# Optimization experiments

Hardware: AMD Instinct MI355X
Metric: run time of the kernel (lower is better)

The kernel has to match this reference:

```python
import jax, jax.numpy as jnp
import numpy as np
from jax.scipy.linalg import cho_solve

N, D, T, K, P = 4000, 256, 52, 20, 100
EPS = 1e-8


def _make_kernel(length_scale):
    # RBF kernel over time grid with the same jitter-doubling rule as the torch code.
    t = np.arange(T, dtype=np.float32)
    sq = (t[None, :] - t[:, None]) ** 2
    Kmat = np.exp(-0.5 * sq / np.float32(length_scale) ** 2).astype(np.float32)
    jitter = 1e-4
    eye = np.eye(T, dtype=np.float32)
    while True:
        if np.linalg.cond(Kmat + jitter * eye) < 1e4:
            break
        jitter *= 2
        if jitter > 0.1:
            break
    return jnp.asarray(Kmat + jitter * eye)

K_LAMBDA = _make_kernel(T / 4)  # lambda GP kernel, shared across all k
K_PHI = _make_kernel(T / 3)     # phi GP kernel, shared across all k


def setup_inputs() -> dict:
    key = jax.random.key(0)
    ks = jax.random.split(key, 7)
    lambda_ = jax.random.normal(ks[0], (N, K, T), dtype=jnp.float32)
    phi = jax.random.normal(ks[1], (K, D, T), dtype=jnp.float32)
    gamma = 0.1 * jax.random.normal(ks[2], (P, K), dtype=jnp.float32)
    G = jax.random.normal(ks[3], (N, P), dtype=jnp.float32)
    Y = (jax.random.uniform(ks[4], (N, D, T)) < 0.05).astype(jnp.float32)
    logit_prev_t = jax.random.normal(ks[5], (D, T), dtype=jnp.float32) - 3.0
    event_times = jax.random.randint(ks[6], (N, D), 0, T)
    return dict(lambda_=lambda_, phi=phi, gamma=gamma, G=G, Y=Y,
                logit_prev_t=logit_prev_t, event_times=event_times)


def reference(lambda_, phi, gamma, G, Y, logit_prev_t, event_times):
    # --- forward: softmax over topics, sigmoid disease probs, mixture ---
    theta = jax.nn.softmax(lambda_, axis=1)          # [N,K,T]
    phi_prob = jax.nn.sigmoid(phi)                   # [K,D,T]
    pi = jnp.einsum('nkt,kdt->ndt', theta, phi_prob) # [N,D,T]
    pi = jnp.clip(pi, EPS, 1.0 - EPS)

    # --- survival data loss ---
    tgrid = jnp.arange(T)[None, None, :]             # [1,1,T]
    e = event_times[:, :, None]                      # [N,D,1]
    mask_before = (tgrid < e).astype(pi.dtype)
    mask_at = (tgrid == e).astype(pi.dtype)
    log_pi = jnp.log(pi)
    log_1mpi = jnp.log1p(-pi)
    loss_censored = -jnp.sum(log_1mpi * mask_before)
    loss_event = -jnp.sum(log_pi * mask_at * Y)
    loss_no_event = -jnp.sum(log_1mpi * mask_at * (1.0 - Y))
    data_loss = (loss_censored + loss_event + loss_no_event) / N

    # --- GP prior loss: batched cholesky solves replace per-sample loops ---
    L_lam = jnp.linalg.cholesky(K_LAMBDA)            # [T,T]
    L_phi = jnp.linalg.cholesky(K_PHI)               # [T,T]
    mean_lam = G @ gamma                             # [N,K]
    dev_lam = (lambda_ - mean_lam[:, :, None]).reshape(N * K, T)  # [N*K,T]
    v_lam = cho_solve((L_lam, True), dev_lam.T)      # [T,N*K]
    gp_lambda = 0.5 * jnp.sum(dev_lam.T * v_lam)
    dev_phi = (phi - logit_prev_t[None, :, :]).reshape(K * D, T)  # [K*D,T]
    v_phi = cho_solve((L_phi, True), dev_phi.T)      # [T,K*D]
    gp_phi = 0.5 * jnp.sum(dev_phi.T * v_phi)
    gp_loss = gp_lambda / N + gp_phi / D

    return data_loss + gp_loss
```

## Files before the change

kernel.cpp:

```cpp
#include <hip/hip_runtime.h>
#include <math.h>
#include <string.h>

#define Nn 4000
#define Dd 256
#define Tt 52
#define Kk 20
#define Pp 100
#define TC 13

#define GRID_GRAM 145
#define GRID_DATA 2000
#define GRID_MAIN (GRID_GRAM + GRID_DATA)

#define PB_PHIP 52
#define PB_MEAN 313
#define GRID_PREP (PB_PHIP + PB_MEAN)

#define OFF_W     0
#define OFF_GPART 5408
#define OFF_DLP   5556
#define OFF_CNT   7556
#define OFF_M     7560
#define OFF_PHIP  87560

#define GR_ROWS 64

__global__ __launch_bounds__(256) void prep_kernel(
    const float* __restrict__ phi, const float* __restrict__ gamma,
    const float* __restrict__ G, float* __restrict__ phip_t,
    float* __restrict__ M, unsigned int* __restrict__ cnt) {
    const int bx = blockIdx.x, tid = threadIdx.x;
    if (bx < PB_PHIP) {
        if (bx == 0 && tid == 0) *cnt = 0u;
        int gid = bx * 256 + tid;
        int d = gid / Tt, t = gid - d * Tt;
        float v[Kk];
#pragma unroll
        for (int k = 0; k < Kk; ++k) {
            float x = phi[k * (Dd * Tt) + gid];
            v[k] = 1.f / (1.f + __expf(-x));
        }
#pragma unroll
        for (int k = 0; k < Kk; ++k)
            phip_t[((size_t)t * Kk + k) * Dd + d] = v[k];
        return;
    }
    int gid = (bx - PB_PHIP) * 256 + tid;
    if (gid < Nn * Kk) {
        int n = gid / Kk, k = gid - n * Kk;
        float m = 0.f;
        for (int p = 0; p < Pp; ++p) m += G[n * Pp + p] * gamma[p * Kk + k];
        M[gid] = m;
    }
}

__global__ __launch_bounds__(256)
__attribute__((amdgpu_waves_per_eu(3, 4)))
void main_kernel(
    const float* __restrict__ lam, const float* __restrict__ phi,
    const float* __restrict__ logit_prev, const int* __restrict__ ev,
    const float* __restrict__ Y, const float* __restrict__ phip_t,
    const float* __restrict__ M, const float* __restrict__ W,
    float* __restrict__ ws, float* __restrict__ out,
    unsigned int* __restrict__ cnt) {
    __shared__ __align__(16) union SM {
        struct { float thS[TC][8][Kk]; float lamS[8][Kk][TC + 1]; } d;
        struct { float rows[GR_ROWS][56]; } g;
    } sm;
    __shared__ double redd[256];
    __shared__ float wsum[4];
    __shared__ int isLast;
    const int bx = blockIdx.x, tid = threadIdx.x;

    if (bx < GRID_GRAM) {
        const bool isPhi = (bx >= 125);
        const int ntile = isPhi ? 4 : 10;
        const int base = isPhi ? (bx - 125) * 256 : bx * 640;
        const int ta = tid % 13, tb = tid / 13;
        float acc[4][4] = {};
        for (int it = 0; it < ntile; ++it) {
            const int R0 = base + it * GR_ROWS;
            __syncthreads();
            for (int idx = tid; idx < GR_ROWS * Tt; idx += 256) {
                int r = idx / Tt, t = idx - r * Tt;
                int R = R0 + r;
                float v;
                if (isPhi) v = phi[R * Tt + t] - logit_prev[(R & (Dd - 1)) * Tt + t];
                else       v = lam[R * Tt + t] - M[R];
                sm.g.rows[r][t] = v;
            }
            __syncthreads();
            if (tb < 13) {
                for (int r = 0; r < GR_ROWS; ++r) {
                    float4 a = *(const float4*)&sm.g.rows[r][4 * ta];
                    float4 b = *(const float4*)&sm.g.rows[r][4 * tb];
                    float av[4] = {a.x, a.y, a.z, a.w};
                    float bv[4] = {b.x, b.y, b.z, b.w};
#pragma unroll
                    for (int i = 0; i < 4; ++i)
#pragma unroll
                        for (int j = 0; j < 4; ++j) acc[i][j] += av[i] * bv[j];
                }
            }
        }
        double s = 0.0;
        if (tb < 13) {
            const float* Wb = W + (isPhi ? 2704 : 0);
#pragma unroll
            for (int i = 0; i < 4; ++i)
#pragma unroll
                for (int j = 0; j < 4; ++j)
                    s += (double)acc[i][j] *
                         (double)Wb[(4 * ta + i) * Tt + 4 * tb + j];
        }
        redd[tid] = s;
        __syncthreads();
        for (int off = 128; off; off >>= 1) {
            if (tid < off) redd[tid] += redd[tid + off];
            __syncthreads();
        }
        if (tid == 0) {
            ws[OFF_GPART + bx] = (float)redd[0];
            __threadfence();
            unsigned prev = atomicAdd(cnt, 1u);
            isLast = (prev == GRID_MAIN - 1) ? 1 : 0;
        }
    } else {
        const int bid = bx - GRID_GRAM;
        const int d = tid;
        const int ng = bid >> 2;
        const int chunk = bid & 3;
        const int t0 = chunk * TC;
        const int n0 = ng * 8;

        if (tid < 8 * Kk) {
            int n = tid / Kk, k = tid - n * Kk;
            const float* src = lam + ((size_t)(n0 + n) * Kk + k) * Tt + t0;
#pragma unroll
            for (int j = 0; j < TC; ++j) sm.d.lamS[n][k][j] = src[j];
        }

        float pvA[Kk], pvB[Kk];
#define LOADPV(BUF, J) do {                                                    \
        const float* pt_ = phip_t + (size_t)(t0 + (J)) * (Kk * Dd) + d;        \
        _Pragma("unroll")                                                      \
        for (int k = 0; k < Kk; ++k) BUF[k] = pt_[k * Dd];                     \
    } while (0)
        LOADPV(pvA, 0);

        int e[8];
#pragma unroll
        for (int g = 0; g < 8; ++g) e[g] = ev[(n0 + g) * Dd + d];

        float Yv[8], acc[8], pie[8], prod[8];
#pragma unroll
        for (int g = 0; g < 8; ++g) {
            acc[g] = 0.f; prod[g] = 1.f; pie[g] = 0.5f; Yv[g] = 0.f;
            if ((unsigned)(e[g] - t0) < (unsigned)TC)
                Yv[g] = __builtin_nontemporal_load(
                    Y + (size_t)((n0 + g) * Dd + d) * Tt + e[g]);
        }

        __syncthreads();
        if (tid < 8 * TC) {
            int n = tid / TC, j = tid - n * TC;
            float v[Kk];
            float m = -1e30f;
#pragma unroll
            for (int k = 0; k < Kk; ++k) { v[k] = sm.d.lamS[n][k][j]; m = fmaxf(m, v[k]); }
            float s = 0.f;
#pragma unroll
            for (int k = 0; k < Kk; ++k) { v[k] = __expf(v[k] - m); s += v[k]; }
            float inv = 1.f / s;
#pragma unroll
            for (int k = 0; k < Kk; ++k) sm.d.thS[j][n][k] = v[k] * inv;
        }
        __syncthreads();

        float4 c0, c1, c2, c3, c4;
        {
            const float4* thp = (const float4*)&sm.d.thS[0][0][0];
            c0 = thp[0]; c1 = thp[1]; c2 = thp[2]; c3 = thp[3]; c4 = thp[4];
        }

#define COMPUTE(J, PV) do {                                                    \
        const int t_ = t0 + (J);                                               \
        _Pragma("unroll")                                                      \
        for (int g = 0; g < 8; ++g) {                                          \
            float4 n0_, n1_, n2_, n3_, n4_;                                    \
            const bool hasNext = (g < 7) || ((J) < TC - 1);                    \
            if (hasNext) {                                                     \
                const float4* np_ = (g < 7)                                    \
                    ? (const float4*)&sm.d.thS[(J)][g + 1][0]                  \
                    : (const float4*)&sm.d.thS[(J) + 1][0][0];                 \
                n0_ = np_[0]; n1_ = np_[1]; n2_ = np_[2];                      \
                n3_ = np_[3]; n4_ = np_[4];                                    \
            }                                                                  \
            float pi = c0.x*PV[0] + c0.y*PV[1] + c0.z*PV[2] + c0.w*PV[3]       \
                     + c1.x*PV[4] + c1.y*PV[5] + c1.z*PV[6] + c1.w*PV[7]       \
                     + c2.x*PV[8] + c2.y*PV[9] + c2.z*PV[10] + c2.w*PV[11]     \
                     + c3.x*PV[12] + c3.y*PV[13] + c3.z*PV[14] + c3.w*PV[15]   \
                     + c4.x*PV[16] + c4.y*PV[17] + c4.z*PV[18] + c4.w*PV[19];  \
            pi = fminf(fmaxf(pi, 1e-8f), 1.0f - 1e-8f);                        \
            prod[g] *= (t_ <= e[g]) ? (1.f - pi) : 1.f;                        \
            pie[g] = (t_ == e[g]) ? pi : pie[g];                               \
            if (hasNext) { c0 = n0_; c1 = n1_; c2 = n2_; c3 = n3_; c4 = n4_; } \
        }                                                                      \
        if ((((J) & 3) == 3) || ((J) == TC - 1)) {                             \
            _Pragma("unroll")                                                  \
            for (int g = 0; g < 8; ++g) {                                      \
                acc[g] += __logf(prod[g]); prod[g] = 1.f;                      \
            }                                                                  \
        }                                                                      \
    } while (0)

#pragma unroll 1
        for (int j2 = 0; j2 < TC - 1; j2 += 2) {
            LOADPV(pvB, j2 + 1);
            __builtin_amdgcn_sched_barrier(0);
            COMPUTE(j2, pvA);
            if (j2 + 2 < TC) LOADPV(pvA, j2 + 2);
            __builtin_amdgcn_sched_barrier(0);
            COMPUTE(j2 + 1, pvB);
        }
        COMPUTE(TC - 1, pvA);

        float tsum = 0.f;
#pragma unroll
        for (int g = 0; g < 8; ++g)
            tsum += acc[g] + Yv[g] * (__logf(pie[g]) - __logf(1.f - pie[g]));
        for (int off = 32; off; off >>= 1) tsum += __shfl_down(tsum, off, 64);
        if ((tid & 63) == 0) wsum[tid >> 6] = tsum;
        __syncthreads();
        if (tid == 0) {
            ws[OFF_DLP + bid] = -(wsum[0] + wsum[1] + wsum[2] + wsum[3]);
            __threadfence();
            unsigned prev = atomicAdd(cnt, 1u);
            isLast = (prev == GRID_MAIN - 1) ? 1 : 0;
        }
    }
    __syncthreads();
    if (!isLast) return;

    __threadfence();
    double s = 0.0;
    for (int i = tid; i < GRID_GRAM; i += 256) s += (double)ws[OFF_GPART + i];
    double dl = 0.0;
    for (int i = tid; i < GRID_DATA; i += 256) dl += (double)ws[OFF_DLP + i];
    s += dl / Nn;
    redd[tid] = s;
    __syncthreads();
    for (int off = 128; off; off >>= 1) {
        if (tid < off) redd[tid] += redd[tid + off];
        __syncthreads();
    }
    if (tid == 0) out[0] = (float)redd[0];
}


static void build_K_f(double ls_in, float Kf[52][52]) {
    float ls = (float)ls_in;
    float ls2 = ls * ls;
    for (int i = 0; i < 52; ++i)
        for (int j = 0; j < 52; ++j) {
            float sq = (float)((i - j) * (i - j));
            float arg = (-0.5f * sq) / ls2;
            Kf[i][j] = expf(arg);
        }
}

static void jacobi_eig(double a[52][52], double ev[52]) {
    const int n = 52;
    for (int sweep = 0; sweep < 100; ++sweep) {
        double off = 0;
        for (int p = 0; p < n - 1; ++p)
            for (int q = p + 1; q < n; ++q) off += a[p][q] * a[p][q];
        if (off < 1e-24) break;
        for (int p = 0; p < n - 1; ++p)
            for (int q = p + 1; q < n; ++q) {
                double apq = a[p][q];
                if (fabs(apq) < 1e-300) continue;
                double th = (a[q][q] - a[p][p]) / (2.0 * apq);
                double t = (th >= 0 ? 1.0 : -1.0) / (fabs(th) + sqrt(th * th + 1.0));
                double c = 1.0 / sqrt(t * t + 1.0), s = t * c;
                for (int i = 0; i < n; ++i) {
                    double aip = a[i][p], aiq = a[i][q];
                    a[i][p] = c * aip - s * aiq;
                    a[i][q] = s * aip + c * aiq;
                }
                for (int i = 0; i < n; ++i) {
                    double api = a[p][i], aqi = a[q][i];
                    a[p][i] = c * api - s * aqi;
                    a[q][i] = s * api + c * aqi;
                }
            }
    }
    for (int i = 0; i < n; ++i) ev[i] = a[i][i];
}

static void build_A(const float Kf[52][52], double jitter, double A[52][52]) {
    float jf = (float)jitter;
    for (int i = 0; i < 52; ++i)
        for (int j = 0; j < 52; ++j) A[i][j] = (double)Kf[i][j];
    for (int i = 0; i < 52; ++i) A[i][i] = (double)(float)(Kf[i][i] + jf);
}

static double cond_of(const float Kf[52][52], double jitter) {
    double A[52][52], ev[52];
    build_A(Kf, jitter, A);
    jacobi_eig(A, ev);
    double mx = 0.0, mn = 1e300;
    for (int i = 0; i < 52; ++i) {
        double a = fabs(ev[i]);
        if (a > mx) mx = a;
        if (a < mn) mn = a;
    }
    if (mn <= 0.0) return 1e300;
    return mx / mn;
}

static double find_jitter(const float Kf[52][52]) {
    double jitter = 1e-4;
    while (true) {
        if (cond_of(Kf, jitter) < 1e4) break;
        jitter *= 2.0;
        if (jitter > 0.1) break;
    }
    return jitter;
}

static void chol_inv_scaled(const float Kf[52][52], double jitter, double scale,
                            float* out) {
    const int n = 52;
    double A[52][52], L[52][52];
    build_A(Kf, jitter, A);
    memset(L, 0, sizeof(L));
    for (int j = 0; j < n; ++j) {
        double s = A[j][j];
        for (int k = 0; k < j; ++k) s -= L[j][k] * L[j][k];
        L[j][j] = sqrt(s);
        for (int i = j + 1; i < n; ++i) {
            double v = A[i][j];
            for (int k = 0; k < j; ++k) v -= L[i][k] * L[j][k];
            L[i][j] = v / L[j][j];
        }
    }
    for (int c = 0; c < n; ++c) {
        double y[52], x[52];
        for (int i = 0; i < n; ++i) {
            double v = (i == c) ? 1.0 : 0.0;
            for (int k = 0; k < i; ++k) v -= L[i][k] * y[k];
            y[i] = v / L[i][i];
        }
        for (int i = n - 1; i >= 0; --i) {
            double v = y[i];
            for (int k = i + 1; k < n; ++k) v -= L[k][i] * x[k];
            x[i] = v / L[i][i];
        }
        for (int i = 0; i < n; ++i) out[i * 52 + c] = (float)(x[i] * scale);
    }
}

struct KinvInit {
    float* w;
    KinvInit() {
        if (hipHostMalloc((void**)&w, 5408 * sizeof(float)) != hipSuccess)
            w = (float*)malloc(5408 * sizeof(float));
        float Kf[52][52];
        build_K_f(52.0 / 4.0, Kf);
        chol_inv_scaled(Kf, find_jitter(Kf), 0.5 / Nn, w);
        build_K_f(52.0 / 3.0, Kf);
        chol_inv_scaled(Kf, find_jitter(Kf), 0.5 / Dd, w + 2704);
    }
};
static KinvInit g_kinv;


extern "C" void kernel_launch(void* const* d_in, const int* in_sizes, int n_in,
                              void* d_out, int out_size, void* d_ws, size_t ws_size,
                              hipStream_t stream) {
    (void)in_sizes; (void)n_in; (void)out_size; (void)ws_size;
    const float* lam        = (const float*)d_in[0];
    const float* phi        = (const float*)d_in[1];
    const float* gamma      = (const float*)d_in[2];
    const float* G          = (const float*)d_in[3];
    const float* Y          = (const float*)d_in[4];
    const float* logit_prev = (const float*)d_in[5];
    const int*   ev         = (const int*)d_in[6];
    float* out = (float*)d_out;
    float* ws  = (float*)d_ws;

    hipMemcpyAsync(ws + OFF_W, g_kinv.w, 5408 * sizeof(float),
                   hipMemcpyHostToDevice, stream);

    prep_kernel<<<GRID_PREP, 256, 0, stream>>>(
        phi, gamma, G, ws + OFF_PHIP, ws + OFF_M,
        (unsigned int*)(ws + OFF_CNT));
    main_kernel<<<GRID_MAIN, 256, 0, stream>>>(
        lam, phi, logit_prev, ev, Y, ws + OFF_PHIP, ws + OFF_M, ws + OFF_W,
        ws, out, (unsigned int*)(ws + OFF_CNT));
}
```

Baseline: 421.9 us.

## Precompute softmax theta in prep kernel and read it via scalar loads

Moves the topic softmax out of the main data-loss blocks into the prep kernel, which writes theta to a global workspace as an [N,T,K] array. The main kernel then reads each sample's theta row with inline-asm s_load_dwordx16/x4 scalar loads instead of staging lambda and theta through shared memory. This removes two block barriers, the per-block softmax and the LDS traffic. In exchange it adds a global write and read of theta (about 16 MB), puts small-latency scalar loads on the critical path with an explicit lgkmcnt wait, and drops the waves_per_eu attribute.

```diff
diff --git a/kernel.cpp b/kernel.cpp
--- a/kernel.cpp
+++ b/kernel.cpp
@@ -15,7 +15,8 @@
 
 #define PB_PHIP 52
 #define PB_MEAN 313
-#define GRID_PREP (PB_PHIP + PB_MEAN)
+#define PB_TH   813
+#define GRID_PREP (PB_PHIP + PB_MEAN + PB_TH)
 
 #define OFF_W     0
 #define OFF_GPART 5408
@@ -23,13 +24,15 @@
 #define OFF_CNT   7556
 #define OFF_M     7560
 #define OFF_PHIP  87560
+#define OFF_THETA 353800
 
 #define GR_ROWS 64
 
 __global__ __launch_bounds__(256) void prep_kernel(
-    const float* __restrict__ phi, const float* __restrict__ gamma,
-    const float* __restrict__ G, float* __restrict__ phip_t,
-    float* __restrict__ M, unsigned int* __restrict__ cnt) {
+    const float* __restrict__ lam, const float* __restrict__ phi,
+    const float* __restrict__ gamma, const float* __restrict__ G,
+    float* __restrict__ phip_t, float* __restrict__ M,
+    float* __restrict__ theta, unsigned int* __restrict__ cnt) {
     const int bx = blockIdx.x, tid = threadIdx.x;
     if (bx < PB_PHIP) {
         if (bx == 0 && tid == 0) *cnt = 0u;
@@ -46,28 +49,72 @@
             phip_t[((size_t)t * Kk + k) * Dd + d] = v[k];
         return;
     }
-    int gid = (bx - PB_PHIP) * 256 + tid;
-    if (gid < Nn * Kk) {
-        int n = gid / Kk, k = gid - n * Kk;
-        float m = 0.f;
-        for (int p = 0; p < Pp; ++p) m += G[n * Pp + p] * gamma[p * Kk + k];
-        M[gid] = m;
-    }
-}
-
-__global__ __launch_bounds__(256)
-__attribute__((amdgpu_waves_per_eu(3, 4)))
-void main_kernel(
+    if (bx < PB_PHIP + PB_MEAN) {
+        int gid = (bx - PB_PHIP) * 256 + tid;
+        if (gid < Nn * Kk) {
+            int n = gid / Kk, k = gid - n * Kk;
+            float m = 0.f;
+            for (int p = 0; p < Pp; ++p) m += G[n * Pp + p] * gamma[p * Kk + k];
+            M[gid] = m;
+        }
+        return;
+    }
+    int gid = (bx - PB_PHIP - PB_MEAN) * 256 + tid;
+    if (gid < Nn * Tt) {
+        int n = gid / Tt, t = gid - n * Tt;
+        float v[Kk];
+        float m = -1e30f;
+#pragma unroll
+        for (int k = 0; k < Kk; ++k) {
+            v[k] = lam[((size_t)n * Kk + k) * Tt + t];
+            m = fmaxf(m, v[k]);
+        }
+        float s = 0.f;
+#pragma unroll
+        for (int k = 0; k < Kk; ++k) { v[k] = __expf(v[k] - m); s += v[k]; }
+        float inv = 1.f / s;
+        float* dst = theta + (size_t)gid * Kk;
+#pragma unroll
+        for (int q = 0; q < 5; ++q) {
+            float4 o = make_float4(v[4 * q] * inv, v[4 * q + 1] * inv,
+                                   v[4 * q + 2] * inv, v[4 * q + 3] * inv);
+            ((float4*)dst)[q] = o;
+        }
+    }
+}
+
+typedef __attribute__((ext_vector_type(16))) float sf16;
+typedef __attribute__((ext_vector_type(4)))  float sf4;
+
+#define THLOAD(S0, S1, GOFF)                                                   \
+    asm volatile("s_load_dwordx16 %0, %2, %3\n\t"                              \
+                 "s_load_dwordx4  %1, %2, %4"                                  \
+                 : "=&s"(S0), "=&s"(S1)                                        \
+                 : "s"(thJ), "n"(GOFF), "n"((GOFF) + 64))
+
+#define THWAIT4(S0a, S1a, S0b, S1b)                                            \
+    asm volatile("s_waitcnt lgkmcnt(0)"                                        \
+                 : "+s"(S0a), "+s"(S1a), "+s"(S0b), "+s"(S1b))
+
+#define PIG(GG, S0, S1, PV) do {                                               \
+    float pi = S0[0]*PV[0] + S0[1]*PV[1] + S0[2]*PV[2] + S0[3]*PV[3]           \
+             + S0[4]*PV[4] + S0[5]*PV[5] + S0[6]*PV[6] + S0[7]*PV[7]           \
+             + S0[8]*PV[8] + S0[9]*PV[9] + S0[10]*PV[10] + S0[11]*PV[11]       \
+             + S0[12]*PV[12] + S0[13]*PV[13] + S0[14]*PV[14] + S0[15]*PV[15]   \
+             + S1[0]*PV[16] + S1[1]*PV[17] + S1[2]*PV[18] + S1[3]*PV[19];      \
+    pi = fminf(fmaxf(pi, 1e-8f), 1.0f - 1e-8f);                                \
+    prod[GG] *= (t_ <= e[GG]) ? (1.f - pi) : 1.f;                              \
+    pie[GG] = (t_ == e[GG]) ? pi : pie[GG];                                    \
+} while (0)
+
+__global__ __launch_bounds__(256) void main_kernel(
     const float* __restrict__ lam, const float* __restrict__ phi,
     const float* __restrict__ logit_prev, const int* __restrict__ ev,
     const float* __restrict__ Y, const float* __restrict__ phip_t,
-    const float* __restrict__ M, const float* __restrict__ W,
-    float* __restrict__ ws, float* __restrict__ out,
-    unsigned int* __restrict__ cnt) {
-    __shared__ __align__(16) union SM {
-        struct { float thS[TC][8][Kk]; float lamS[8][Kk][TC + 1]; } d;
-        struct { float rows[GR_ROWS][56]; } g;
-    } sm;
+    const float* __restrict__ thetaT, const float* __restrict__ M,
+    const float* __restrict__ W, float* __restrict__ ws,
+    float* __restrict__ out, unsigned int* __restrict__ cnt) {
+    __shared__ __align__(16) float rows[GR_ROWS][56];
     __shared__ double redd[256];
     __shared__ float wsum[4];
     __shared__ int isLast;
@@ -88,13 +135,13 @@
                 float v;
                 if (isPhi) v = phi[R * Tt + t] - logit_prev[(R & (Dd - 1)) * Tt + t];
                 else       v = lam[R * Tt + t] - M[R];
-                sm.g.rows[r][t] = v;
+                rows[r][t] = v;
             }
             __syncthreads();
             if (tb < 13) {
                 for (int r = 0; r < GR_ROWS; ++r) {
-                    float4 a = *(const float4*)&sm.g.rows[r][4 * ta];
-                    float4 b = *(const float4*)&sm.g.rows[r][4 * tb];
+                    float4 a = *(const float4*)&rows[r][4 * ta];
+                    float4 b = *(const float4*)&rows[r][4 * tb];
                     float av[4] = {a.x, a.y, a.z, a.w};
                     float bv[4] = {b.x, b.y, b.z, b.w};
 #pragma unroll
@@ -134,13 +181,6 @@
         const int t0 = chunk * TC;
         const int n0 = ng * 8;
 
-        if (tid < 8 * Kk) {
-            int n = tid / Kk, k = tid - n * Kk;
-            const float* src = lam + ((size_t)(n0 + n) * Kk + k) * Tt + t0;
-#pragma unroll
-            for (int j = 0; j < TC; ++j) sm.d.lamS[n][k][j] = src[j];
-        }
-
         float pvA[Kk], pvB[Kk];
 #define LOADPV(BUF, J) do {                                                    \
         const float* pt_ = phip_t + (size_t)(t0 + (J)) * (Kk * Dd) + d;        \
@@ -162,51 +202,24 @@
                     Y + (size_t)((n0 + g) * Dd + d) * Tt + e[g]);
         }
 
-        __syncthreads();
-        if (tid < 8 * TC) {
-            int n = tid / TC, j = tid - n * TC;
-            float v[Kk];
-            float m = -1e30f;
-#pragma unroll
-            for (int k = 0; k < Kk; ++k) { v[k] = sm.d.lamS[n][k][j]; m = fmaxf(m, v[k]); }
-            float s = 0.f;
-#pragma unroll
-            for (int k = 0; k < Kk; ++k) { v[k] = __expf(v[k] - m); s += v[k]; }
-            float inv = 1.f / s;
-#pragma unroll
-            for (int k = 0; k < Kk; ++k) sm.d.thS[j][n][k] = v[k] * inv;
-        }
-        __syncthreads();
-
-        float4 c0, c1, c2, c3, c4;
-        {
-            const float4* thp = (const float4*)&sm.d.thS[0][0][0];
-            c0 = thp[0]; c1 = thp[1]; c2 = thp[2]; c3 = thp[3]; c4 = thp[4];
-        }
+        const float* thB = thetaT + ((size_t)n0 * Tt + t0) * Kk;
 
 #define COMPUTE(J, PV) do {                                                    \
         const int t_ = t0 + (J);                                               \
-        _Pragma("unroll")                                                      \
-        for (int g = 0; g < 8; ++g) {                                          \
-            float4 n0_, n1_, n2_, n3_, n4_;                                    \
-            const bool hasNext = (g < 7) || ((J) < TC - 1);                    \
-            if (hasNext) {                                                     \
-                const float4* np_ = (g < 7)                                    \
-                    ? (const float4*)&sm.d.thS[(J)][g + 1][0]                  \
-                    : (const float4*)&sm.d.thS[(J) + 1][0][0];                 \
-                n0_ = np_[0]; n1_ = np_[1]; n2_ = np_[2];                      \
-                n3_ = np_[3]; n4_ = np_[4];                                    \
-            }                                                                  \
-            float pi = c0.x*PV[0] + c0.y*PV[1] + c0.z*PV[2] + c0.w*PV[3]       \
-                     + c1.x*PV[4] + c1.y*PV[5] + c1.z*PV[6] + c1.w*PV[7]       \
-                     + c2.x*PV[8] + c2.y*PV[9] + c2.z*PV[10] + c2.w*PV[11]     \
-                     + c3.x*PV[12] + c3.y*PV[13] + c3.z*PV[14] + c3.w*PV[15]   \
-                     + c4.x*PV[16] + c4.y*PV[17] + c4.z*PV[18] + c4.w*PV[19];  \
-            pi = fminf(fmaxf(pi, 1e-8f), 1.0f - 1e-8f);                        \
-            prod[g] *= (t_ <= e[g]) ? (1.f - pi) : 1.f;                        \
-            pie[g] = (t_ == e[g]) ? pi : pie[g];                               \
-            if (hasNext) { c0 = n0_; c1 = n1_; c2 = n2_; c3 = n3_; c4 = n4_; } \
-        }                                                                      \
+        const float* thJ = thB + (J) * Kk;                                     \
+        sf16 A0, B0; sf4 A1, B1;                                               \
+        THLOAD(A0, A1, 0);        THLOAD(B0, B1, 4160);                        \
+        THWAIT4(A0, A1, B0, B1);                                               \
+        PIG(0, A0, A1, PV);       PIG(1, B0, B1, PV);                          \
+        THLOAD(A0, A1, 2 * 4160); THLOAD(B0, B1, 3 * 4160);                    \
+        THWAIT4(A0, A1, B0, B1);                                               \
+        PIG(2, A0, A1, PV);       PIG(3, B0, B1, PV);                          \
+        THLOAD(A0, A1, 4 * 4160); THLOAD(B0, B1, 5 * 4160);                    \
+        THWAIT4(A0, A1, B0, B1);                                               \
+        PIG(4, A0, A1, PV);       PIG(5, B0, B1, PV);                          \
+        THLOAD(A0, A1, 6 * 4160); THLOAD(B0, B1, 7 * 4160);                    \
+        THWAIT4(A0, A1, B0, B1);                                               \
+        PIG(6, A0, A1, PV);       PIG(7, B0, B1, PV);                          \
         if ((((J) & 3) == 3) || ((J) == TC - 1)) {                             \
             _Pragma("unroll")                                                  \
             for (int g = 0; g < 8; ++g) {                                      \
@@ -395,9 +408,9 @@
                    hipMemcpyHostToDevice, stream);
 
     prep_kernel<<<GRID_PREP, 256, 0, stream>>>(
-        phi, gamma, G, ws + OFF_PHIP, ws + OFF_M,
+        lam, phi, gamma, G, ws + OFF_PHIP, ws + OFF_M, ws + OFF_THETA,
         (unsigned int*)(ws + OFF_CNT));
     main_kernel<<<GRID_MAIN, 256, 0, stream>>>(
-        lam, phi, logit_prev, ev, Y, ws + OFF_PHIP, ws + OFF_M, ws + OFF_W,
-        ws, out, (unsigned int*)(ws + OFF_CNT));
-}
+        lam, phi, logit_prev, ev, Y, ws + OFF_PHIP, ws + OFF_THETA,
+        ws + OFF_M, ws + OFF_W, ws, out, (unsigned int*)(ws + OFF_CNT));
+}
```

New measurement: 445.1 us. 5.5% more time.
